# Kernel tuning notes

Measured on AMD Instinct MI355X. Metric: run time of the kernel, lower is better.

## Reference

```python
import jax, jax.numpy as jnp
import numpy as np

NUM_HEADS = 16
BLOCK_SIZE = 64


def setup_inputs() -> dict:
    key = jax.random.key(0)
    ks = jax.random.split(key, 5)
    B, S, C = 2, 2047, 1024
    return {
        "x": jax.random.normal(ks[0], (B, S, C), dtype=jnp.float32),
        "global_token": jax.random.normal(ks[1], (1, 1, C), dtype=jnp.float32),
        "qkv_w": jax.random.normal(ks[2], (3 * C, C), dtype=jnp.float32) * 0.02,
        "proj_w": jax.random.normal(ks[3], (C, C), dtype=jnp.float32) * 0.02,
        "proj_b": jax.random.normal(ks[4], (C,), dtype=jnp.float32) * 0.02,
    }


def reference(x, global_token, qkv_w, proj_w, proj_b):
    B, S, C = x.shape
    H = NUM_HEADS
    D = C // H
    scale = D ** -0.5
    # prepend global token -> N = S + 1
    g = jnp.broadcast_to(global_token, (B, 1, C))
    xg = jnp.concatenate([g, x], axis=1)
    N = S + 1
    # fused qkv projection (torch Linear: x @ W^T)
    qkv = (xg @ qkv_w.T).reshape(B, N, 3, H, D)
    qkv = jnp.transpose(qkv, (2, 0, 3, 1, 4))  # [3, B, H, N, D]
    q, k, v = qkv[0], qkv[1], qkv[2]
    # block-causal mask: query t sees key j iff block(j) <= block(t)
    blk = jnp.arange(N) // BLOCK_SIZE
    mask = blk[:, None] >= blk[None, :]  # [N, N]
    attn = jnp.einsum("bhqd,bhkd->bhqk", q, k) * scale
    attn = jnp.where(mask[None, None], attn, -jnp.inf)
    attn = jax.nn.softmax(attn, axis=-1)
    out = jnp.einsum("bhqk,bhkd->bhqd", attn, v)
    out = jnp.transpose(out, (0, 2, 1, 3)).reshape(B, N, C)
    out = out[:, 1:, :]  # drop global token
    return out @ proj_w.T + proj_b
```

## Files before the change

kernel.cpp:

```cpp
#include <hip/hip_runtime.h>
#include <math.h>

typedef _Float16 h16;
typedef _Float16 half8 __attribute__((ext_vector_type(8)));
typedef _Float16 half4 __attribute__((ext_vector_type(4)));
typedef float f32x4 __attribute__((ext_vector_type(4)));

#define NB 2
#define NS 2047
#define NC 1024
#define NN 2048
#define NH 16
#define ND 64

__device__ __forceinline__ void gl_lds16(const h16* g, h16* l) {
  __builtin_amdgcn_global_load_lds((const __attribute__((address_space(1))) void*)g,
                                   (__attribute__((address_space(3))) void*)l, 16, 0, 0);
}
__device__ __forceinline__ f32x4 mfma32(half8 a, half8 b, f32x4 c) {
  return __builtin_amdgcn_mfma_f32_16x16x32_f16(a, b, c, 0, 0, 0);
}
__device__ __forceinline__ f32x4 mfma16x(half4 a, half4 b, f32x4 c) {
  return __builtin_amdgcn_mfma_f32_16x16x16f16(a, b, c, 0, 0, 0);
}

__global__ __launch_bounds__(256) void cast_all_k(
    const float* __restrict__ x, const float* __restrict__ g,
    const float* __restrict__ qw, const float* __restrict__ pw, h16* __restrict__ out) {
  const size_t i = ((size_t)blockIdx.x * 256 + threadIdx.x) * 8;
  const float* src;
  if (i < (size_t)NB * NN * NC) {
    const int c = (int)(i & (NC - 1));
    const int n = (int)((i >> 10) & (NN - 1));
    const int b = (int)(i >> 21);
    src = (n == 0) ? (g + c) : (x + ((size_t)b * NS + (n - 1)) * NC + c);
  } else {
    const size_t j = i - (size_t)NB * NN * NC;
    src = (j < (size_t)3 * NC * NC) ? (qw + j) : (pw + (j - (size_t)3 * NC * NC));
  }
  float4 f0 = ((const float4*)src)[0];
  float4 f1 = ((const float4*)src)[1];
  h16 tmp[8];
  tmp[0] = (h16)f0.x; tmp[1] = (h16)f0.y; tmp[2] = (h16)f0.z; tmp[3] = (h16)f0.w;
  tmp[4] = (h16)f1.x; tmp[5] = (h16)f1.y; tmp[6] = (h16)f1.z; tmp[7] = (h16)f1.w;
  *(half8*)(out + i) = *(half8*)&tmp[0];
}

__global__ __launch_bounds__(256) void gemm_qkv_h(
    const h16* __restrict__ A, const h16* __restrict__ W, h16* __restrict__ out) {
  __shared__ h16 As[128 * 64];
  __shared__ h16 Bs[128 * 64];
  const int tid = threadIdx.x;
  const int m0 = blockIdx.y * 128, j0 = blockIdx.x * 128;
  const int wid = tid >> 6, lane = tid & 63, l15 = lane & 15, quad = lane >> 4;
  const int rl = lane >> 3, cp = lane & 7, csw = cp ^ rl;
  const h16* ag = A + (size_t)(m0 + wid * 32 + rl) * NC + csw * 8;
  const h16* bg = W + (size_t)(j0 + wid * 32 + rl) * NC + csw * 8;
  f32x4 acc[2][8];
#pragma unroll
  for (int rt = 0; rt < 2; ++rt)
#pragma unroll
    for (int ct = 0; ct < 8; ++ct) acc[rt][ct] = (f32x4){0.f, 0.f, 0.f, 0.f};

  for (int k0 = 0; k0 < NC; k0 += 64) {
    __syncthreads();
#pragma unroll
    for (int i = 0; i < 4; ++i) {
      gl_lds16(ag + (size_t)i * 8 * NC + k0, &As[(wid * 32 + i * 8) * 64]);
      gl_lds16(bg + (size_t)i * 8 * NC + k0, &Bs[(wid * 32 + i * 8) * 64]);
    }
    __syncthreads();
#pragma unroll
    for (int ks = 0; ks < 2; ++ks) {
      const int p0 = ((ks * 4 + quad) ^ (l15 & 7)) * 8;
      half8 af0 = *(const half8*)&As[(wid * 32 + l15) * 64 + p0];
      half8 af1 = *(const half8*)&As[(wid * 32 + 16 + l15) * 64 + p0];
#pragma unroll
      for (int ct = 0; ct < 8; ++ct) {
        half8 bf = *(const half8*)&Bs[(ct * 16 + l15) * 64 + p0];
        acc[0][ct] = mfma32(af0, bf, acc[0][ct]);
        acc[1][ct] = mfma32(af1, bf, acc[1][ct]);
      }
    }
  }
#pragma unroll
  for (int rt = 0; rt < 2; ++rt)
#pragma unroll
    for (int ct = 0; ct < 8; ++ct)
#pragma unroll
      for (int r = 0; r < 4; ++r) {
        const int mm = m0 + wid * 32 + rt * 16 + quad * 4 + r;
        const int jj = j0 + ct * 16 + l15;
        out[(size_t)mm * (3 * NC) + jj] = (h16)acc[rt][ct][r];
      }
}

__global__ __launch_bounds__(256) void kvpack_k(
    const h16* __restrict__ qkvh, h16* __restrict__ kP, h16* __restrict__ vP) {
  __shared__ h16 ts[64 * 72];
  const int kb = blockIdx.x, h = blockIdx.y, b = blockIdx.z;
  const int bh = b * NH + h;
  const int t = threadIdx.x;
  {
    const int r = t >> 2, c = (t & 3) * 16;
    const h16* src = qkvh + ((size_t)(b * NN + kb * 64 + r) * 3 + 1) * NC + h * ND + c;
    half8 k0 = *(const half8*)src;
    half8 k1 = *(const half8*)(src + 8);
    h16* dst = kP + ((size_t)bh * NN + kb * 64 + r) * ND + c;
    *(half8*)dst = k0;
    *(half8*)(dst + 8) = k1;
  }
  {
    const int key = t >> 2, co = (t & 3) * 16;
    const h16* src = qkvh + ((size_t)(b * NN + kb * 64 + key) * 3 + 2) * NC + h * ND + co;
    half8 v0 = *(const half8*)src;
    half8 v1 = *(const half8*)(src + 8);
    *(half8*)&ts[key * 72 + co] = v0;
    *(half8*)&ts[key * 72 + co + 8] = v1;
  }
  __syncthreads();
  {
    const int w = t >> 6, d = t & 63;
    h16 buf[16];
#pragma unroll
    for (int kk = 0; kk < 16; ++kk) buf[kk] = ts[(w * 16 + kk) * 72 + d];
    h16* dst = vP + ((size_t)(bh * 32 + kb) * 4 + w) * 1024 + d * 16;
    *(half8*)dst = *(half8*)&buf[0];
    *(half8*)(dst + 8) = *(half8*)&buf[8];
  }
}

__global__ __launch_bounds__(256, 3) void attn_h(
    const h16* __restrict__ qkvh, const h16* __restrict__ kP,
    const h16* __restrict__ vP, h16* __restrict__ outp) {
  __shared__ float RED[2 * 64 * 36];
  __shared__ float DEN[4 * 64];
  const int bx = blockIdx.x;
  const int qb = 31 - (bx >> 5);
  const int bh = bx & 31;
  const int b = bh >> 4, h = bh & 15;
  const int tid = threadIdx.x, w = tid >> 6, lane = tid & 63;
  const int l15 = lane & 15, quad = lane >> 4;

  half8 bq[4][2];
#pragma unroll
  for (int nt = 0; nt < 4; ++nt) {
    const h16* qp = qkvh + (size_t)(b * NN + qb * 64 + nt * 16 + l15) * (3 * NC) + h * ND + quad * 8;
    bq[nt][0] = (*(const half8*)qp) * (h16)0.125f;
    bq[nt][1] = (*(const half8*)(qp + 32)) * (h16)0.125f;
  }
  const h16* kbase = kP + ((size_t)bh * NN + w * 16 + l15) * ND + quad * 8;
  const h16* vbase = vP + ((size_t)bh * 32 * 4 + w) * 1024 + l15 * 16 + quad * 4;

  f32x4 o[4][4];
  float den[4] = {0.f, 0.f, 0.f, 0.f};
#pragma unroll
  for (int mt = 0; mt < 4; ++mt)
#pragma unroll
    for (int nt = 0; nt < 4; ++nt) o[mt][nt] = (f32x4){0.f, 0.f, 0.f, 0.f};

  half8 kf0 = *(const half8*)kbase;
  half8 kf1 = *(const half8*)(kbase + 32);
  half4 vf0 = *(const half4*)(vbase);
  half4 vf1 = *(const half4*)(vbase + 256);
  half4 vf2 = *(const half4*)(vbase + 512);
  half4 vf3 = *(const half4*)(vbase + 768);

  for (int kb = 0; kb <= qb; ++kb) {
    const int nkb = (kb < qb) ? kb + 1 : kb;
    const h16* kn = kbase + (size_t)nkb * 64 * ND;
    const h16* vn = vbase + (size_t)nkb * 4096;
    half8 nk0 = *(const half8*)kn;
    half8 nk1 = *(const half8*)(kn + 32);
    half4 nv0 = *(const half4*)(vn);
    half4 nv1 = *(const half4*)(vn + 256);
    half4 nv2 = *(const half4*)(vn + 512);
    half4 nv3 = *(const half4*)(vn + 768);
#pragma unroll
    for (int nt = 0; nt < 4; ++nt) {
      f32x4 s = (f32x4){0.f, 0.f, 0.f, 0.f};
      s = mfma32(kf0, bq[nt][0], s);
      s = mfma32(kf1, bq[nt][1], s);
      float e0 = __expf(s[0]), e1 = __expf(s[1]);
      float e2 = __expf(s[2]), e3 = __expf(s[3]);
      den[nt] += (e0 + e1) + (e2 + e3);
      int2 pi;
      pi.x = __builtin_bit_cast(int, __builtin_amdgcn_cvt_pkrtz(e0, e1));
      pi.y = __builtin_bit_cast(int, __builtin_amdgcn_cvt_pkrtz(e2, e3));
      half4 p = __builtin_bit_cast(half4, pi);
      o[0][nt] = mfma16x(vf0, p, o[0][nt]);
      o[1][nt] = mfma16x(vf1, p, o[1][nt]);
      o[2][nt] = mfma16x(vf2, p, o[2][nt]);
      o[3][nt] = mfma16x(vf3, p, o[3][nt]);
    }
    kf0 = nk0; kf1 = nk1;
    vf0 = nv0; vf1 = nv1; vf2 = nv2; vf3 = nv3;
  }

#pragma unroll
  for (int nt = 0; nt < 4; ++nt) {
    den[nt] += __shfl_xor(den[nt], 16);
    den[nt] += __shfl_xor(den[nt], 32);
  }
  __syncthreads();
  if (quad == 0) {
#pragma unroll
    for (int nt = 0; nt < 4; ++nt) DEN[w * 64 + nt * 16 + l15] = den[nt];
  }
#pragma unroll
  for (int r = 0; r < 2; ++r) {
    if (r) __syncthreads();
    if (w < 2) {
#pragma unroll
      for (int mt2 = 0; mt2 < 2; ++mt2)
#pragma unroll
        for (int nt = 0; nt < 4; ++nt)
          *(f32x4*)&RED[(w * 64 + nt * 16 + l15) * 36 + mt2 * 16 + quad * 4] =
              o[r * 2 + mt2][nt];
    }
    __syncthreads();
    if (w >= 2) {
#pragma unroll
      for (int mt2 = 0; mt2 < 2; ++mt2)
#pragma unroll
        for (int nt = 0; nt < 4; ++nt) {
          float* p = &RED[((w - 2) * 64 + nt * 16 + l15) * 36 + mt2 * 16 + quad * 4];
          f32x4 t = *(f32x4*)p;
          *(f32x4*)p = t + o[r * 2 + mt2][nt];
        }
    }
    __syncthreads();
    {
      const int q = w * 16 + l15;
      const float dt = DEN[q] + DEN[64 + q] + DEN[128 + q] + DEN[192 + q];
      const float inv = 1.f / dt;
      f32x4 x0 = *(const f32x4*)&RED[(0 * 64 + q) * 36 + quad * 8];
      f32x4 x1 = *(const f32x4*)&RED[(0 * 64 + q) * 36 + quad * 8 + 4];
      f32x4 y0 = *(const f32x4*)&RED[(1 * 64 + q) * 36 + quad * 8];
      f32x4 y1 = *(const f32x4*)&RED[(1 * 64 + q) * 36 + quad * 8 + 4];
      x0 += y0;
      x1 += y1;
      int4 pk;
      pk.x = __builtin_bit_cast(int, __builtin_amdgcn_cvt_pkrtz(x0[0] * inv, x0[1] * inv));
      pk.y = __builtin_bit_cast(int, __builtin_amdgcn_cvt_pkrtz(x0[2] * inv, x0[3] * inv));
      pk.z = __builtin_bit_cast(int, __builtin_amdgcn_cvt_pkrtz(x1[0] * inv, x1[1] * inv));
      pk.w = __builtin_bit_cast(int, __builtin_amdgcn_cvt_pkrtz(x1[2] * inv, x1[3] * inv));
      h16* op = outp + (size_t)(b * NN + qb * 64 + q) * NC + h * ND + r * 32 + quad * 8;
      *(half8*)op = __builtin_bit_cast(half8, pk);
    }
  }
}

__global__ __launch_bounds__(256) void gemm_proj_h(
    const h16* __restrict__ Ah, const h16* __restrict__ W,
    const float* __restrict__ bias, float* __restrict__ out) {
  __shared__ h16 As[64 * 64];
  __shared__ h16 Bs[128 * 64];
  const int tid = threadIdx.x;
  const int m0 = blockIdx.y * 64, j0 = blockIdx.x * 128;
  const int wid = tid >> 6, lane = tid & 63, l15 = lane & 15, quad = lane >> 4;
  const int rl = lane >> 3, csw = (lane & 7) ^ rl;
  const h16* ag[2];
#pragma unroll
  for (int i = 0; i < 2; ++i) {
    int m = m0 + wid * 16 + i * 8 + rl;
    if (m > NB * NS - 1) m = NB * NS - 1;
    const int bb = (m >= NS) ? 1 : 0;
    ag[i] = Ah + (size_t)(bb * NN + m - bb * NS + 1) * NC + csw * 8;
  }
  const h16* bg = W + (size_t)(j0 + wid * 32 + rl) * NC + csw * 8;
  f32x4 acc[8];
#pragma unroll
  for (int ct = 0; ct < 8; ++ct) acc[ct] = (f32x4){0.f, 0.f, 0.f, 0.f};

  for (int k0 = 0; k0 < NC; k0 += 64) {
    __syncthreads();
    gl_lds16(ag[0] + k0, &As[(wid * 16) * 64]);
    gl_lds16(ag[1] + k0, &As[(wid * 16 + 8) * 64]);
#pragma unroll
    for (int i = 0; i < 4; ++i)
      gl_lds16(bg + (size_t)i * 8 * NC + k0, &Bs[(wid * 32 + i * 8) * 64]);
    __syncthreads();
#pragma unroll
    for (int ks = 0; ks < 2; ++ks) {
      const int p0 = ((ks * 4 + quad) ^ (l15 & 7)) * 8;
      half8 af = *(const half8*)&As[(wid * 16 + l15) * 64 + p0];
#pragma unroll
      for (int ct = 0; ct < 8; ++ct) {
        half8 bf = *(const half8*)&Bs[(ct * 16 + l15) * 64 + p0];
        acc[ct] = mfma32(af, bf, acc[ct]);
      }
    }
  }
#pragma unroll
  for (int ct = 0; ct < 8; ++ct) {
    const float bv = bias[j0 + ct * 16 + l15];
#pragma unroll
    for (int r = 0; r < 4; ++r) {
      const int mm = m0 + wid * 16 + quad * 4 + r;
      if (mm < NB * NS)
        out[(size_t)mm * NC + j0 + ct * 16 + l15] = acc[ct][r] + bv;
    }
  }
}

extern "C" void kernel_launch(void* const* d_in, const int* in_sizes, int n_in,
                              void* d_out, int out_size, void* d_ws, size_t ws_size,
                              hipStream_t stream) {
  const float* x = (const float*)d_in[0];
  const float* g = (const float*)d_in[1];
  const float* qkv_w = (const float*)d_in[2];
  const float* proj_w = (const float*)d_in[3];
  const float* proj_b = (const float*)d_in[4];
  float* out = (float*)d_out;

  h16* xgh  = (h16*)d_ws;
  h16* w3h  = xgh + (size_t)NB * NN * NC;
  h16* wph  = w3h + (size_t)3 * NC * NC;
  h16* qkvh = wph + (size_t)NC * NC;
  h16* kPb  = qkvh + (size_t)NB * NN * 3 * NC;
  h16* vPb  = kPb + (size_t)NB * NH * NN * ND;
  h16* attnh = vPb + (size_t)NB * NH * NN * ND;

  cast_all_k<<<dim3(4096), 256, 0, stream>>>(x, g, qkv_w, proj_w, xgh);
  gemm_qkv_h<<<dim3(24, 32), 256, 0, stream>>>(xgh, w3h, qkvh);
  kvpack_k<<<dim3(32, NH, NB), 256, 0, stream>>>(qkvh, kPb, vPb);
  attn_h<<<dim3(1024), 256, 0, stream>>>(qkvh, kPb, vPb, attnh);
  gemm_proj_h<<<dim3(8, 64), 256, 0, stream>>>(attnh, wph, proj_b, out);
}
```

Baseline: 175.9 us.

## Fuse K/V packing into QKV GEMM epilogue and raise MFMA priority in attention

The QKV GEMM epilogue now writes Q and K straight into per-head [B,H,N,D] layouts. V tiles are staged through shared memory with an XOR swizzle and written in the transposed packed layout that attention expects. This removes the separate kvpack kernel launch and the round trip through the interleaved qkv buffer. Separately, the attention inner loop raises wave priority around the MFMA/exp section using s_setprio. The trade-off is more scattered strided stores in the GEMM epilogue for Q/K, plus an extra LDS pass for the V blocks.

```diff
diff --git a/kernel.cpp b/kernel.cpp
--- a/kernel.cpp
+++ b/kernel.cpp
@@ -47,9 +47,11 @@
 }
 
 __global__ __launch_bounds__(256) void gemm_qkv_h(
-    const h16* __restrict__ A, const h16* __restrict__ W, h16* __restrict__ out) {
-  __shared__ h16 As[128 * 64];
-  __shared__ h16 Bs[128 * 64];
+    const h16* __restrict__ A, const h16* __restrict__ W,
+    h16* __restrict__ qP, h16* __restrict__ kP, h16* __restrict__ vP) {
+  __shared__ h16 SM[128 * 128];
+  h16* As = SM;
+  h16* Bs = SM + 128 * 64;
   const int tid = threadIdx.x;
   const int m0 = blockIdx.y * 128, j0 = blockIdx.x * 128;
   const int wid = tid >> 6, lane = tid & 63, l15 = lane & 15, quad = lane >> 4;
@@ -83,55 +85,59 @@
       }
     }
   }
-#pragma unroll
-  for (int rt = 0; rt < 2; ++rt)
-#pragma unroll
-    for (int ct = 0; ct < 8; ++ct)
-#pragma unroll
-      for (int r = 0; r < 4; ++r) {
-        const int mm = m0 + wid * 32 + rt * 16 + quad * 4 + r;
-        const int jj = j0 + ct * 16 + l15;
-        out[(size_t)mm * (3 * NC) + jj] = (h16)acc[rt][ct][r];
+
+  const int b = m0 >> 11, n0 = m0 & (NN - 1);
+  if (j0 < 2 * NC) {
+    h16* base = (j0 < NC) ? qP : kP;
+    const int coff = (j0 < NC) ? 0 : NC;
+#pragma unroll
+    for (int rt = 0; rt < 2; ++rt)
+#pragma unroll
+      for (int ct = 0; ct < 8; ++ct) {
+        const int col = j0 - coff + ct * 16 + l15;
+        const int h = col >> 6, d = col & 63;
+        h16* dst = base + (((size_t)(b * NH + h)) * NN + n0) * ND + d;
+#pragma unroll
+        for (int r = 0; r < 4; ++r) {
+          const int mloc = wid * 32 + rt * 16 + quad * 4 + r;
+          dst[(size_t)mloc * ND] = (h16)acc[rt][ct][r];
+        }
       }
-}
-
-__global__ __launch_bounds__(256) void kvpack_k(
-    const h16* __restrict__ qkvh, h16* __restrict__ kP, h16* __restrict__ vP) {
-  __shared__ h16 ts[64 * 72];
-  const int kb = blockIdx.x, h = blockIdx.y, b = blockIdx.z;
-  const int bh = b * NH + h;
-  const int t = threadIdx.x;
-  {
-    const int r = t >> 2, c = (t & 3) * 16;
-    const h16* src = qkvh + ((size_t)(b * NN + kb * 64 + r) * 3 + 1) * NC + h * ND + c;
-    half8 k0 = *(const half8*)src;
-    half8 k1 = *(const half8*)(src + 8);
-    h16* dst = kP + ((size_t)bh * NN + kb * 64 + r) * ND + c;
-    *(half8*)dst = k0;
-    *(half8*)(dst + 8) = k1;
-  }
-  {
-    const int key = t >> 2, co = (t & 3) * 16;
-    const h16* src = qkvh + ((size_t)(b * NN + kb * 64 + key) * 3 + 2) * NC + h * ND + co;
-    half8 v0 = *(const half8*)src;
-    half8 v1 = *(const half8*)(src + 8);
-    *(half8*)&ts[key * 72 + co] = v0;
-    *(half8*)&ts[key * 72 + co + 8] = v1;
-  }
-  __syncthreads();
-  {
-    const int w = t >> 6, d = t & 63;
-    h16 buf[16];
-#pragma unroll
-    for (int kk = 0; kk < 16; ++kk) buf[kk] = ts[(w * 16 + kk) * 72 + d];
-    h16* dst = vP + ((size_t)(bh * 32 + kb) * 4 + w) * 1024 + d * 16;
-    *(half8*)dst = *(half8*)&buf[0];
-    *(half8*)(dst + 8) = *(half8*)&buf[8];
+  } else {
+    __syncthreads();
+#pragma unroll
+    for (int rt = 0; rt < 2; ++rt)
+#pragma unroll
+      for (int ct = 0; ct < 8; ++ct)
+#pragma unroll
+        for (int r = 0; r < 4; ++r) {
+          const int mloc = wid * 32 + rt * 16 + quad * 4 + r;
+          const int jloc = ct * 16 + l15;
+          SM[mloc * 128 + (jloc ^ (((mloc >> 2) & 3) << 3))] = (h16)acc[rt][ct][r];
+        }
+    __syncthreads();
+    const int kb0 = n0 >> 6;
+    const int h0 = (j0 - 2 * NC) >> 6;
+    const int w = tid >> 6, d = tid & 63;
+#pragma unroll
+    for (int u = 0; u < 4; ++u) {
+      const int kbl = u >> 1, hl = u & 1;
+      const int bh = b * NH + h0 + hl;
+      h16 buf[16];
+#pragma unroll
+      for (int kk = 0; kk < 16; ++kk) {
+        const int row = kbl * 64 + w * 16 + kk;
+        buf[kk] = SM[row * 128 + ((hl * 64 + d) ^ (((row >> 2) & 3) << 3))];
+      }
+      h16* dst = vP + ((size_t)(bh * 32 + kb0 + kbl) * 4 + w) * 1024 + d * 16;
+      *(half8*)dst = *(half8*)&buf[0];
+      *(half8*)(dst + 8) = *(half8*)&buf[8];
+    }
   }
 }
 
 __global__ __launch_bounds__(256, 3) void attn_h(
-    const h16* __restrict__ qkvh, const h16* __restrict__ kP,
+    const h16* __restrict__ qP, const h16* __restrict__ kP,
     const h16* __restrict__ vP, h16* __restrict__ outp) {
   __shared__ float RED[2 * 64 * 36];
   __shared__ float DEN[4 * 64];
@@ -145,7 +151,7 @@
   half8 bq[4][2];
 #pragma unroll
   for (int nt = 0; nt < 4; ++nt) {
-    const h16* qp = qkvh + (size_t)(b * NN + qb * 64 + nt * 16 + l15) * (3 * NC) + h * ND + quad * 8;
+    const h16* qp = qP + ((size_t)bh * NN + qb * 64 + nt * 16 + l15) * ND + quad * 8;
     bq[nt][0] = (*(const half8*)qp) * (h16)0.125f;
     bq[nt][1] = (*(const half8*)(qp + 32)) * (h16)0.125f;
   }
@@ -176,6 +182,7 @@
     half4 nv1 = *(const half4*)(vn + 256);
     half4 nv2 = *(const half4*)(vn + 512);
     half4 nv3 = *(const half4*)(vn + 768);
+    __builtin_amdgcn_s_setprio(1);
 #pragma unroll
     for (int nt = 0; nt < 4; ++nt) {
       f32x4 s = (f32x4){0.f, 0.f, 0.f, 0.f};
@@ -193,6 +200,7 @@
       o[2][nt] = mfma16x(vf2, p, o[2][nt]);
       o[3][nt] = mfma16x(vf3, p, o[3][nt]);
     }
+    __builtin_amdgcn_s_setprio(0);
     kf0 = nk0; kf1 = nk1;
     vf0 = nv0; vf1 = nv1; vf2 = nv2; vf3 = nv3;
   }
@@ -317,14 +325,13 @@
   h16* xgh  = (h16*)d_ws;
   h16* w3h  = xgh + (size_t)NB * NN * NC;
   h16* wph  = w3h + (size_t)3 * NC * NC;
-  h16* qkvh = wph + (size_t)NC * NC;
-  h16* kPb  = qkvh + (size_t)NB * NN * 3 * NC;
-  h16* vPb  = kPb + (size_t)NB * NH * NN * ND;
-  h16* attnh = vPb + (size_t)NB * NH * NN * ND;
+  h16* qP   = wph + (size_t)NC * NC;
+  h16* kP   = qP + (size_t)NB * NH * NN * ND;
+  h16* vP   = kP + (size_t)NB * NH * NN * ND;
+  h16* attnh = vP + (size_t)NB * NH * NN * ND;
 
   cast_all_k<<<dim3(4096), 256, 0, stream>>>(x, g, qkv_w, proj_w, xgh);
-  gemm_qkv_h<<<dim3(24, 32), 256, 0, stream>>>(xgh, w3h, qkvh);
-  kvpack_k<<<dim3(32, NH, NB), 256, 0, stream>>>(qkvh, kPb, vPb);
-  attn_h<<<dim3(1024), 256, 0, stream>>>(qkvh, kPb, vPb, attnh);
+  gemm_qkv_h<<<dim3(24, 32), 256, 0, stream>>>(xgh, w3h, qP, kP, vP);
+  attn_h<<<dim3(1024), 256, 0, stream>>>(qP, kP, vP, attnh);
   gemm_proj_h<<<dim3(8, 64), 256, 0, stream>>>(attnh, wph, proj_b, out);
 }
```

Measured after the change: 174.4 us. About the same (-0.8%).
